# Optimization experiments

Measured on AMD Instinct MI355X. Metric: run time of the kernel, lower is better.

Reference implementation:

```python
import jax, jax.numpy as jnp
import numpy as np

EPS = 1e-5

def setup_inputs() -> dict:
    key = jax.random.key(0)
    k1, k2 = jax.random.split(key)
    N, D, O = 32768, 4096, 256
    x = jax.random.normal(k1, (N, D), dtype=jnp.float32)
    gamma = jnp.ones((D,), dtype=jnp.float32)
    beta = jnp.zeros((D,), dtype=jnp.float32)
    W = jax.random.normal(k2, (O, D), dtype=jnp.float32) * (1.0 / np.sqrt(D))
    b = jnp.zeros((O,), dtype=jnp.float32)
    return {"x": x, "gamma": gamma, "beta": beta, "W": W, "b": b}


def reference(x, gamma, beta, W, b):
    # BatchNorm1d in training mode: per-feature batch mean and biased variance
    mean = jnp.mean(x, axis=0)                      # [D]
    var = jnp.mean(jnp.square(x - mean), axis=0)    # [D], biased (divide by N)
    xhat = (x - mean) * jax.lax.rsqrt(var + EPS)
    h = jax.nn.relu(xhat * gamma + beta)            # [N, D]
    # Linear projection
    return h @ W.T + b                               # [N, O]
```

## Files before the change

kernel.cpp:

```cpp
#include <hip/hip_runtime.h>
#include <hip/hip_bf16.h>

#define NROWS 32768
#define DDIM  4096
#define ODIM  256
#define EPSV  1e-5f

#define CHUNKS 128
#define RPC    256

#define BM 128
#define BK 64
#define NKT (DDIM / BK)

typedef __attribute__((ext_vector_type(4))) float          f32x4;
typedef __attribute__((ext_vector_type(8))) __bf16         bf16x8;
typedef __attribute__((ext_vector_type(8))) unsigned short u16x8;
typedef __attribute__((ext_vector_type(4))) unsigned short u16x4;

static __device__ __forceinline__ unsigned short f2bf(float f) {
  return __builtin_bit_cast(unsigned short, __float2bfloat16(f));
}

__global__ __launch_bounds__(256) void k1_stats(const float* __restrict__ x,
                                                float* __restrict__ psum,
                                                float* __restrict__ psq) {
  const int col = blockIdx.x * 1024 + threadIdx.x * 4;
  const float* p = x + (size_t)blockIdx.y * RPC * DDIM + col;
  f32x4 s = {0.f, 0.f, 0.f, 0.f};
  f32x4 q = {0.f, 0.f, 0.f, 0.f};
#pragma unroll 8
  for (int r = 0; r < RPC; ++r) {
    f32x4 v = *(const f32x4*)p;
    p += DDIM;
    s += v;
    q += v * v;
  }
  *(f32x4*)(psum + (size_t)blockIdx.y * DDIM + col) = s;
  *(f32x4*)(psq  + (size_t)blockIdx.y * DDIM + col) = q;
}

__global__ __launch_bounds__(256) void k2_stats_finalize(
    const float* __restrict__ psum, const float* __restrict__ psq,
    const float* __restrict__ gamma, const float* __restrict__ beta,
    float* __restrict__ scale, float* __restrict__ shift) {
  __shared__ float ss[4][64];
  __shared__ float sq[4][64];
  const int lane = threadIdx.x & 63;
  const int g    = threadIdx.x >> 6;
  const int d    = blockIdx.x * 64 + lane;
  float s = 0.f, qq = 0.f;
  for (int c = g * 32; c < (g + 1) * 32; ++c) {
    s  += psum[(size_t)c * DDIM + d];
    qq += psq [(size_t)c * DDIM + d];
  }
  ss[g][lane] = s;
  sq[g][lane] = qq;
  __syncthreads();
  if (g == 0) {
    s  = ss[0][lane] + ss[1][lane] + ss[2][lane] + ss[3][lane];
    qq = sq[0][lane] + sq[1][lane] + sq[2][lane] + sq[3][lane];
    const float inv = 1.0f / (float)NROWS;
    const float mean = s * inv;
    const float var  = fmaxf(qq * inv - mean * mean, 0.f);
    const float a = gamma[d] * rsqrtf(var + EPSV);
    scale[d] = a;
    shift[d] = beta[d] - mean * a;
  }
}

__global__ __launch_bounds__(256) void k2_wconv(const float* __restrict__ Wf,
                                                unsigned short* __restrict__ Wb) {
  const size_t i = ((size_t)blockIdx.x * 256 + threadIdx.x) * 4;
  f32x4 v = *(const f32x4*)(Wf + i);
  u16x4 o;
  o[0] = f2bf(v[0]); o[1] = f2bf(v[1]); o[2] = f2bf(v[2]); o[3] = f2bf(v[3]);
  *(u16x4*)(Wb + i) = o;
}

__global__ __launch_bounds__(512, 1) void k3_bn_gemm(
    const float* __restrict__ x,
    const unsigned short* __restrict__ Wb,
    const float* __restrict__ scale,
    const float* __restrict__ shift,
    const float* __restrict__ bias,
    float* __restrict__ out) {
  __shared__ unsigned short As[2][BM * BK];
  __shared__ unsigned short Bs[2][ODIM * BK];
  __shared__ float SF[DDIM];
  __shared__ float SH[DDIM];

  const int tid = threadIdx.x;
  const int l   = tid & 63;
  const int w   = tid >> 6;
  const int wr  = w >> 2;
  const int wc  = w & 3;
  const size_t bm0 = (size_t)blockIdx.x * BM;

  ((f32x4*)SF)[tid * 2]     = ((const f32x4*)scale)[tid * 2];
  ((f32x4*)SF)[tid * 2 + 1] = ((const f32x4*)scale)[tid * 2 + 1];
  ((f32x4*)SH)[tid * 2]     = ((const f32x4*)shift)[tid * 2];
  ((f32x4*)SH)[tid * 2 + 1] = ((const f32x4*)shift)[tid * 2 + 1];

  const int rA = tid >> 3;
  const int uA = tid & 7;
  const float* xp0 = x + (bm0 + rA) * (size_t)DDIM + uA * 8;
  const float* xp1 = xp0 + (size_t)64 * DDIM;
  const int awo = rA * 64 + ((uA ^ (rA & 7)) << 3);
  int ktb = uA * 8;

  const unsigned short* bsrc[4];
#pragma unroll
  for (int q = 0; q < 4; ++q) {
    const int p  = w * 256 + q * 64 + l;
    const int o  = p >> 3;
    const int up = p & 7;
    bsrc[q] = Wb + (size_t)o * DDIM + ((up ^ (o & 7)) << 3);
  }

  int offA[4], offB[4];
#pragma unroll
  for (int i = 0; i < 4; ++i) {
    const int row = wr * 64 + i * 16 + (l & 15);
    offA[i] = row * 64 + (((l >> 4) ^ (row & 7)) << 3);
  }
#pragma unroll
  for (int j = 0; j < 4; ++j) {
    const int row = wc * 64 + j * 16 + (l & 15);
    offB[j] = row * 64 + (((l >> 4) ^ (row & 7)) << 3);
  }

  const f32x4 zero = {0.f, 0.f, 0.f, 0.f};
  f32x4 acc[4][4];
#pragma unroll
  for (int i = 0; i < 4; ++i)
#pragma unroll
    for (int j = 0; j < 4; ++j) acc[i][j] = zero;

#define ISSUE_A(V00, V01, V10, V11)                                            \
  asm volatile("global_load_dwordx4 %0, %1, off" : "=v"(V00) : "v"(xp0));      \
  asm volatile("global_load_dwordx4 %0, %1, off" : "=v"(V01) : "v"(xp0 + 4));  \
  asm volatile("global_load_dwordx4 %0, %1, off" : "=v"(V10) : "v"(xp1));      \
  asm volatile("global_load_dwordx4 %0, %1, off" : "=v"(V11) : "v"(xp1 + 4));  \
  asm volatile("" ::: "memory");

#define ISSUE_B(BUFI)                                                          \
  _Pragma("unroll")                                                            \
  for (int q = 0; q < 4; ++q) {                                                \
    __builtin_amdgcn_global_load_lds(                                          \
        (__attribute__((address_space(1))) void*)bsrc[q],                      \
        (__attribute__((address_space(3))) void*)(                             \
            &Bs[BUFI][(w * 256 + q * 64) * 8]),                                \
        16, 0, 0);                                                             \
    bsrc[q] += BK;                                                             \
  }

#define TRANSFORM_WRITE(BUFI, V00, V01, V10, V11)                              \
  {                                                                            \
    f32x4 sa0 = *(const f32x4*)&SF[ktb];                                       \
    f32x4 sa1 = *(const f32x4*)&SF[ktb + 4];                                   \
    f32x4 sc0 = *(const f32x4*)&SH[ktb];                                       \
    f32x4 sc1 = *(const f32x4*)&SH[ktb + 4];                                   \
    ktb += BK;                                                                 \
    u16x8 pk0, pk1;                                                            \
    _Pragma("unroll")                                                          \
    for (int e = 0; e < 4; ++e) {                                              \
      pk0[e]     = f2bf(fmaxf(V00[e] * sa0[e] + sc0[e], 0.f));                 \
      pk0[e + 4] = f2bf(fmaxf(V01[e] * sa1[e] + sc1[e], 0.f));                 \
      pk1[e]     = f2bf(fmaxf(V10[e] * sa0[e] + sc0[e], 0.f));                 \
      pk1[e + 4] = f2bf(fmaxf(V11[e] * sa1[e] + sc1[e], 0.f));                 \
    }                                                                          \
    *(u16x8*)&As[BUFI][awo]        = pk0;                                      \
    *(u16x8*)&As[BUFI][awo + 4096] = pk1;                                      \
  }

#define MFMA_PHASE(BUFI)                                                       \
  _Pragma("unroll")                                                            \
  for (int kk = 0; kk < 2; ++kk) {                                             \
    const int kx = kk << 5;                                                    \
    bf16x8 af[4], bfr[4];                                                      \
    _Pragma("unroll")                                                          \
    for (int i = 0; i < 4; ++i)                                                \
      af[i] = __builtin_bit_cast(bf16x8,                                       \
                                 *(const u16x8*)&As[BUFI][offA[i] ^ kx]);      \
    _Pragma("unroll")                                                          \
    for (int j = 0; j < 4; ++j)                                                \
      bfr[j] = __builtin_bit_cast(bf16x8,                                      \
                                  *(const u16x8*)&Bs[BUFI][offB[j] ^ kx]);     \
    _Pragma("unroll")                                                          \
    for (int i = 0; i < 4; ++i)                                                \
      _Pragma("unroll")                                                        \
      for (int j = 0; j < 4; ++j)                                              \
        acc[i][j] = __builtin_amdgcn_mfma_f32_16x16x32_bf16(                   \
            af[i], bfr[j], acc[i][j], 0, 0, 0);                                \
  }

  {
    f32x4 v00, v01, v10, v11;
    ISSUE_A(v00, v01, v10, v11);
    ISSUE_B(0);
    xp0 += BK; xp1 += BK;
    asm volatile("s_waitcnt lgkmcnt(0)" ::: "memory");
    __builtin_amdgcn_sched_barrier(0);
    __builtin_amdgcn_s_barrier();
    asm volatile("s_waitcnt vmcnt(4)" ::: "memory");
    __builtin_amdgcn_sched_barrier(0);
    TRANSFORM_WRITE(0, v00, v01, v10, v11);
    asm volatile("s_waitcnt vmcnt(0) lgkmcnt(0)" ::: "memory");
    __builtin_amdgcn_sched_barrier(0);
    __builtin_amdgcn_s_barrier();
  }

#define STEP(CUR, PF)                                                          \
  do {                                                                         \
    f32x4 v00, v01, v10, v11;                                                  \
    if (PF) {                                                                  \
      ISSUE_A(v00, v01, v10, v11);                                             \
      ISSUE_B((CUR) ^ 1);                                                      \
      xp0 += BK; xp1 += BK;                                                    \
    }                                                                          \
    MFMA_PHASE(CUR);                                                           \
    if (PF) {                                                                  \
      asm volatile("s_waitcnt vmcnt(4)" ::: "memory");                         \
      __builtin_amdgcn_sched_barrier(0);                                       \
      TRANSFORM_WRITE((CUR) ^ 1, v00, v01, v10, v11);                          \
    }                                                                          \
    asm volatile("s_waitcnt vmcnt(0) lgkmcnt(0)" ::: "memory");                \
    __builtin_amdgcn_sched_barrier(0);                                         \
    __builtin_amdgcn_s_barrier();                                              \
  } while (0)

  for (int kt = 0; kt < NKT - 2; kt += 2) {
    STEP(0, true);
    STEP(1, true);
  }
  STEP(0, true);
  STEP(1, false);
#undef STEP
#undef MFMA_PHASE
#undef TRANSFORM_WRITE
#undef ISSUE_B
#undef ISSUE_A

  const int cl = l & 15;
  const int rg = l >> 4;
#pragma unroll
  for (int j = 0; j < 4; ++j) {
    const int oc = wc * 64 + j * 16 + cl;
    const float bv = bias[oc];
#pragma unroll
    for (int i = 0; i < 4; ++i) {
      const size_t r0 = bm0 + wr * 64 + i * 16 + rg * 4;
#pragma unroll
      for (int rr = 0; rr < 4; ++rr) {
        out[(r0 + rr) * ODIM + oc] = acc[i][j][rr] + bv;
      }
    }
  }
}

extern "C" void kernel_launch(void* const* d_in, const int* in_sizes, int n_in,
                              void* d_out, int out_size, void* d_ws, size_t ws_size,
                              hipStream_t stream) {
  const float* x     = (const float*)d_in[0];
  const float* gamma = (const float*)d_in[1];
  const float* beta  = (const float*)d_in[2];
  const float* W     = (const float*)d_in[3];
  const float* b     = (const float*)d_in[4];
  float* out = (float*)d_out;

  float* psum  = (float*)d_ws;
  float* psq   = psum + (size_t)CHUNKS * DDIM;
  float* scale = psum + 2 * (size_t)CHUNKS * DDIM;
  float* shift = scale + DDIM;
  unsigned short* Wb = (unsigned short*)(shift + DDIM);

  k1_stats<<<dim3(4, CHUNKS), 256, 0, stream>>>(x, psum, psq);
  k2_stats_finalize<<<DDIM / 64, 256, 0, stream>>>(psum, psq, gamma, beta, scale, shift);
  k2_wconv<<<(ODIM * DDIM) / 1024, 256, 0, stream>>>(W, Wb);
  k3_bn_gemm<<<NROWS / BM, 512, 0, stream>>>(x, Wb, scale, shift, b, out);
}
```

Measured before the change: 239.2 us.

## Emit bf16 copy of x during stats pass and feed GEMM from it

```diff
diff --git a/kernel.cpp b/kernel.cpp
--- a/kernel.cpp
+++ b/kernel.cpp
@@ -21,12 +21,18 @@
 static __device__ __forceinline__ unsigned short f2bf(float f) {
   return __builtin_bit_cast(unsigned short, __float2bfloat16(f));
 }
+static __device__ __forceinline__ float bf2f(unsigned short u) {
+  return __builtin_bit_cast(float, ((unsigned)u) << 16);
+}
 
 __global__ __launch_bounds__(256) void k1_stats(const float* __restrict__ x,
                                                 float* __restrict__ psum,
-                                                float* __restrict__ psq) {
+                                                float* __restrict__ psq,
+                                                unsigned short* __restrict__ xb) {
   const int col = blockIdx.x * 1024 + threadIdx.x * 4;
-  const float* p = x + (size_t)blockIdx.y * RPC * DDIM + col;
+  const size_t base = (size_t)blockIdx.y * RPC * DDIM + col;
+  const float* p = x + base;
+  unsigned short* xo = xb + base;
   f32x4 s = {0.f, 0.f, 0.f, 0.f};
   f32x4 q = {0.f, 0.f, 0.f, 0.f};
 #pragma unroll 8
@@ -35,6 +41,10 @@
     p += DDIM;
     s += v;
     q += v * v;
+    u16x4 o;
+    o[0] = f2bf(v[0]); o[1] = f2bf(v[1]); o[2] = f2bf(v[2]); o[3] = f2bf(v[3]);
+    *(u16x4*)xo = o;
+    xo += DDIM;
   }
   *(f32x4*)(psum + (size_t)blockIdx.y * DDIM + col) = s;
   *(f32x4*)(psq  + (size_t)blockIdx.y * DDIM + col) = q;
@@ -79,7 +89,7 @@
 }
 
 __global__ __launch_bounds__(512, 1) void k3_bn_gemm(
-    const float* __restrict__ x,
+    const unsigned short* __restrict__ xb,
     const unsigned short* __restrict__ Wb,
     const float* __restrict__ scale,
     const float* __restrict__ shift,
@@ -87,8 +97,8 @@
     float* __restrict__ out) {
   __shared__ unsigned short As[2][BM * BK];
   __shared__ unsigned short Bs[2][ODIM * BK];
-  __shared__ float SF[DDIM];
-  __shared__ float SH[DDIM];
+  __shared__ unsigned short SFb[DDIM];
+  __shared__ unsigned short SHb[DDIM];
 
   const int tid = threadIdx.x;
   const int l   = tid & 63;
@@ -97,17 +107,29 @@
   const int wc  = w & 3;
   const size_t bm0 = (size_t)blockIdx.x * BM;
 
-  ((f32x4*)SF)[tid * 2]     = ((const f32x4*)scale)[tid * 2];
-  ((f32x4*)SF)[tid * 2 + 1] = ((const f32x4*)scale)[tid * 2 + 1];
-  ((f32x4*)SH)[tid * 2]     = ((const f32x4*)shift)[tid * 2];
-  ((f32x4*)SH)[tid * 2 + 1] = ((const f32x4*)shift)[tid * 2 + 1];
-
-  const int rA = tid >> 3;
-  const int uA = tid & 7;
-  const float* xp0 = x + (bm0 + rA) * (size_t)DDIM + uA * 8;
-  const float* xp1 = xp0 + (size_t)64 * DDIM;
-  const int awo = rA * 64 + ((uA ^ (rA & 7)) << 3);
-  int ktb = uA * 8;
+  {
+    const int c0 = tid * 8;
+    f32x4 s0 = *(const f32x4*)(scale + c0);
+    f32x4 s1 = *(const f32x4*)(scale + c0 + 4);
+    f32x4 h0 = *(const f32x4*)(shift + c0);
+    f32x4 h1 = *(const f32x4*)(shift + c0 + 4);
+    u16x8 os, oh;
+#pragma unroll
+    for (int e = 0; e < 4; ++e) {
+      os[e] = f2bf(s0[e]); os[e + 4] = f2bf(s1[e]);
+      oh[e] = f2bf(h0[e]); oh[e + 4] = f2bf(h1[e]);
+    }
+    *(u16x8*)&SFb[c0] = os;
+    *(u16x8*)&SHb[c0] = oh;
+  }
+
+  const int rA = tid >> 2;
+  const int uA = tid & 3;
+  const unsigned short* xp = xb + (bm0 + rA) * (size_t)DDIM + uA * 16;
+  const int sw = rA & 7;
+  const int aw0 = rA * 64 + (((uA * 2)     ^ sw) << 3);
+  const int aw1 = rA * 64 + (((uA * 2 + 1) ^ sw) << 3);
+  int ktb = uA * 16;
 
   const unsigned short* bsrc[4];
 #pragma unroll
@@ -137,11 +159,10 @@
 #pragma unroll
     for (int j = 0; j < 4; ++j) acc[i][j] = zero;
 
-#define ISSUE_A(V00, V01, V10, V11)                                            \
-  asm volatile("global_load_dwordx4 %0, %1, off" : "=v"(V00) : "v"(xp0));      \
-  asm volatile("global_load_dwordx4 %0, %1, off" : "=v"(V01) : "v"(xp0 + 4));  \
-  asm volatile("global_load_dwordx4 %0, %1, off" : "=v"(V10) : "v"(xp1));      \
-  asm volatile("global_load_dwordx4 %0, %1, off" : "=v"(V11) : "v"(xp1 + 4));  \
+#define ISSUE_A(S0, S1)                                                        \
+  asm volatile("global_load_dwordx4 %0, %1, off" : "=v"(S0) : "v"(xp));        \
+  asm volatile("global_load_dwordx4 %0, %1, off" : "=v"(S1) : "v"(xp + 8));    \
+  xp += BK;                                                                    \
   asm volatile("" ::: "memory");
 
 #define ISSUE_B(BUFI)                                                          \
@@ -153,25 +174,24 @@
             &Bs[BUFI][(w * 256 + q * 64) * 8]),                                \
         16, 0, 0);                                                             \
     bsrc[q] += BK;                                                             \
-  }
-
-#define TRANSFORM_WRITE(BUFI, V00, V01, V10, V11)                              \
+  }                                                                            \
+  asm volatile("" ::: "memory");
+
+#define TRANSFORM_WRITE(BUFI, S0, S1)                                          \
   {                                                                            \
-    f32x4 sa0 = *(const f32x4*)&SF[ktb];                                       \
-    f32x4 sa1 = *(const f32x4*)&SF[ktb + 4];                                   \
-    f32x4 sc0 = *(const f32x4*)&SH[ktb];                                       \
-    f32x4 sc1 = *(const f32x4*)&SH[ktb + 4];                                   \
+    u16x8 a0 = *(const u16x8*)&SFb[ktb];                                       \
+    u16x8 a1 = *(const u16x8*)&SFb[ktb + 8];                                   \
+    u16x8 c0 = *(const u16x8*)&SHb[ktb];                                       \
+    u16x8 c1 = *(const u16x8*)&SHb[ktb + 8];                                   \
     ktb += BK;                                                                 \
     u16x8 pk0, pk1;                                                            \
     _Pragma("unroll")                                                          \
-    for (int e = 0; e < 4; ++e) {                                              \
-      pk0[e]     = f2bf(fmaxf(V00[e] * sa0[e] + sc0[e], 0.f));                 \
-      pk0[e + 4] = f2bf(fmaxf(V01[e] * sa1[e] + sc1[e], 0.f));                 \
-      pk1[e]     = f2bf(fmaxf(V10[e] * sa0[e] + sc0[e], 0.f));                 \
-      pk1[e + 4] = f2bf(fmaxf(V11[e] * sa1[e] + sc1[e], 0.f));                 \
+    for (int e = 0; e < 8; ++e) {                                              \
+      pk0[e] = f2bf(fmaxf(bf2f(S0[e]) * bf2f(a0[e]) + bf2f(c0[e]), 0.f));      \
+      pk1[e] = f2bf(fmaxf(bf2f(S1[e]) * bf2f(a1[e]) + bf2f(c1[e]), 0.f));      \
     }                                                                          \
-    *(u16x8*)&As[BUFI][awo]        = pk0;                                      \
-    *(u16x8*)&As[BUFI][awo + 4096] = pk1;                                      \
+    *(u16x8*)&As[BUFI][aw0] = pk0;                                             \
+    *(u16x8*)&As[BUFI][aw1] = pk1;                                             \
   }
 
 #define MFMA_PHASE(BUFI)                                                       \
@@ -196,16 +216,15 @@
   }
 
   {
-    f32x4 v00, v01, v10, v11;
-    ISSUE_A(v00, v01, v10, v11);
+    u16x8 s0, s1;
+    ISSUE_A(s0, s1);
     ISSUE_B(0);
-    xp0 += BK; xp1 += BK;
     asm volatile("s_waitcnt lgkmcnt(0)" ::: "memory");
     __builtin_amdgcn_sched_barrier(0);
     __builtin_amdgcn_s_barrier();
     asm volatile("s_waitcnt vmcnt(4)" ::: "memory");
     __builtin_amdgcn_sched_barrier(0);
-    TRANSFORM_WRITE(0, v00, v01, v10, v11);
+    TRANSFORM_WRITE(0, s0, s1);
     asm volatile("s_waitcnt vmcnt(0) lgkmcnt(0)" ::: "memory");
     __builtin_amdgcn_sched_barrier(0);
     __builtin_amdgcn_s_barrier();
@@ -213,17 +232,16 @@
 
 #define STEP(CUR, PF)                                                          \
   do {                                                                         \
-    f32x4 v00, v01, v10, v11;                                                  \
+    u16x8 s0, s1;                                                              \
     if (PF) {                                                                  \
-      ISSUE_A(v00, v01, v10, v11);                                             \
+      ISSUE_A(s0, s1);                                                         \
       ISSUE_B((CUR) ^ 1);                                                      \
-      xp0 += BK; xp1 += BK;                                                    \
     }                                                                          \
     MFMA_PHASE(CUR);                                                           \
     if (PF) {                                                                  \
       asm volatile("s_waitcnt vmcnt(4)" ::: "memory");                         \
       __builtin_amdgcn_sched_barrier(0);                                       \
-      TRANSFORM_WRITE((CUR) ^ 1, v00, v01, v10, v11);                          \
+      TRANSFORM_WRITE((CUR) ^ 1, s0, s1);                                      \
     }                                                                          \
     asm volatile("s_waitcnt vmcnt(0) lgkmcnt(0)" ::: "memory");                \
     __builtin_amdgcn_sched_barrier(0);                                         \
@@ -269,14 +287,15 @@
   const float* b     = (const float*)d_in[4];
   float* out = (float*)d_out;
 
-  float* psum  = (float*)d_ws;
+  unsigned short* xbw = (unsigned short*)d_ws;
+  float* psum  = (float*)(xbw + (size_t)NROWS * DDIM);
   float* psq   = psum + (size_t)CHUNKS * DDIM;
-  float* scale = psum + 2 * (size_t)CHUNKS * DDIM;
+  float* scale = psq  + (size_t)CHUNKS * DDIM;
   float* shift = scale + DDIM;
   unsigned short* Wb = (unsigned short*)(shift + DDIM);
 
-  k1_stats<<<dim3(4, CHUNKS), 256, 0, stream>>>(x, psum, psq);
+  k1_stats<<<dim3(4, CHUNKS), 256, 0, stream>>>(x, psum, psq, xbw);
   k2_stats_finalize<<<DDIM / 64, 256, 0, stream>>>(psum, psq, gamma, beta, scale, shift);
   k2_wconv<<<(ODIM * DDIM) / 1024, 256, 0, stream>>>(W, Wb);
-  k3_bn_gemm<<<NROWS / BM, 512, 0, stream>>>(x, Wb, scale, shift, b, out);
-}
+  k3_bn_gemm<<<NROWS / BM, 512, 0, stream>>>(xbw, Wb, scale, shift, b, out);
+}
```

Measured after the change: 281.1 us. 17.5% more time.

## Split GEMM output columns across two blocks with XCD-aware mapping and bf16 BN params

Applied to the files above, without the earlier changes.

```diff
diff --git a/kernel.cpp b/kernel.cpp
--- a/kernel.cpp
+++ b/kernel.cpp
@@ -10,6 +10,7 @@
 #define RPC    256
 
 #define BM 128
+#define BN 128
 #define BK 64
 #define NKT (DDIM / BK)
 
@@ -20,6 +21,9 @@
 
 static __device__ __forceinline__ unsigned short f2bf(float f) {
   return __builtin_bit_cast(unsigned short, __float2bfloat16(f));
+}
+static __device__ __forceinline__ float bf2f(unsigned short u) {
+  return __builtin_bit_cast(float, ((unsigned)u) << 16);
 }
 
 __global__ __launch_bounds__(256) void k1_stats(const float* __restrict__ x,
@@ -40,82 +44,91 @@
   *(f32x4*)(psq  + (size_t)blockIdx.y * DDIM + col) = q;
 }
 
-__global__ __launch_bounds__(256) void k2_stats_finalize(
+__global__ __launch_bounds__(256) void k2_finalize_wconv(
     const float* __restrict__ psum, const float* __restrict__ psq,
     const float* __restrict__ gamma, const float* __restrict__ beta,
-    float* __restrict__ scale, float* __restrict__ shift) {
-  __shared__ float ss[4][64];
-  __shared__ float sq[4][64];
-  const int lane = threadIdx.x & 63;
-  const int g    = threadIdx.x >> 6;
-  const int d    = blockIdx.x * 64 + lane;
-  float s = 0.f, qq = 0.f;
-  for (int c = g * 32; c < (g + 1) * 32; ++c) {
-    s  += psum[(size_t)c * DDIM + d];
-    qq += psq [(size_t)c * DDIM + d];
-  }
-  ss[g][lane] = s;
-  sq[g][lane] = qq;
-  __syncthreads();
-  if (g == 0) {
-    s  = ss[0][lane] + ss[1][lane] + ss[2][lane] + ss[3][lane];
-    qq = sq[0][lane] + sq[1][lane] + sq[2][lane] + sq[3][lane];
-    const float inv = 1.0f / (float)NROWS;
-    const float mean = s * inv;
-    const float var  = fmaxf(qq * inv - mean * mean, 0.f);
-    const float a = gamma[d] * rsqrtf(var + EPSV);
-    scale[d] = a;
-    shift[d] = beta[d] - mean * a;
-  }
-}
-
-__global__ __launch_bounds__(256) void k2_wconv(const float* __restrict__ Wf,
-                                                unsigned short* __restrict__ Wb) {
-  const size_t i = ((size_t)blockIdx.x * 256 + threadIdx.x) * 4;
-  f32x4 v = *(const f32x4*)(Wf + i);
-  u16x4 o;
-  o[0] = f2bf(v[0]); o[1] = f2bf(v[1]); o[2] = f2bf(v[2]); o[3] = f2bf(v[3]);
-  *(u16x4*)(Wb + i) = o;
-}
-
-__global__ __launch_bounds__(512, 1) void k3_bn_gemm(
+    const float* __restrict__ Wf,
+    unsigned short* __restrict__ ssb, unsigned short* __restrict__ shb,
+    unsigned short* __restrict__ Wb) {
+  if (blockIdx.x < 64) {
+    __shared__ float ss[4][64];
+    __shared__ float sq[4][64];
+    const int lane = threadIdx.x & 63;
+    const int g    = threadIdx.x >> 6;
+    const int d    = blockIdx.x * 64 + lane;
+    float s = 0.f, qq = 0.f;
+    for (int c = g * 32; c < (g + 1) * 32; ++c) {
+      s  += psum[(size_t)c * DDIM + d];
+      qq += psq [(size_t)c * DDIM + d];
+    }
+    ss[g][lane] = s;
+    sq[g][lane] = qq;
+    __syncthreads();
+    if (g == 0) {
+      s  = ss[0][lane] + ss[1][lane] + ss[2][lane] + ss[3][lane];
+      qq = sq[0][lane] + sq[1][lane] + sq[2][lane] + sq[3][lane];
+      const float inv = 1.0f / (float)NROWS;
+      const float mean = s * inv;
+      const float var  = fmaxf(qq * inv - mean * mean, 0.f);
+      const float a = gamma[d] * rsqrtf(var + EPSV);
+      ssb[d] = f2bf(a);
+      shb[d] = f2bf(beta[d] - mean * a);
+    }
+  } else {
+    const size_t i = ((size_t)(blockIdx.x - 64) * 256 + threadIdx.x) * 4;
+    f32x4 v = *(const f32x4*)(Wf + i);
+    u16x4 o;
+    o[0] = f2bf(v[0]); o[1] = f2bf(v[1]); o[2] = f2bf(v[2]); o[3] = f2bf(v[3]);
+    *(u16x4*)(Wb + i) = o;
+  }
+}
+
+__global__ __launch_bounds__(256, 2) void k3_bn_gemm(
     const float* __restrict__ x,
     const unsigned short* __restrict__ Wb,
-    const float* __restrict__ scale,
-    const float* __restrict__ shift,
+    const unsigned short* __restrict__ ssg,
+    const unsigned short* __restrict__ shg,
     const float* __restrict__ bias,
     float* __restrict__ out) {
   __shared__ unsigned short As[2][BM * BK];
-  __shared__ unsigned short Bs[2][ODIM * BK];
-  __shared__ float SF[DDIM];
-  __shared__ float SH[DDIM];
+  __shared__ unsigned short Bs[2][BN * BK];
+  __shared__ unsigned short SFb[DDIM];
+  __shared__ unsigned short SHb[DDIM];
 
   const int tid = threadIdx.x;
   const int l   = tid & 63;
   const int w   = tid >> 6;
-  const int wr  = w >> 2;
-  const int wc  = w & 3;
-  const size_t bm0 = (size_t)blockIdx.x * BM;
-
-  ((f32x4*)SF)[tid * 2]     = ((const f32x4*)scale)[tid * 2];
-  ((f32x4*)SF)[tid * 2 + 1] = ((const f32x4*)scale)[tid * 2 + 1];
-  ((f32x4*)SH)[tid * 2]     = ((const f32x4*)shift)[tid * 2];
-  ((f32x4*)SH)[tid * 2 + 1] = ((const f32x4*)shift)[tid * 2 + 1];
-
-  const int rA = tid >> 3;
-  const int uA = tid & 7;
-  const float* xp0 = x + (bm0 + rA) * (size_t)DDIM + uA * 8;
-  const float* xp1 = xp0 + (size_t)64 * DDIM;
-  const int awo = rA * 64 + ((uA ^ (rA & 7)) << 3);
-  int ktb = uA * 8;
+  const int wr  = w >> 1;
+  const int wc  = w & 1;
+  const int b   = blockIdx.x;
+  const int xcd = b & 7;
+  const int j8  = b >> 3;
+  const int m   = xcd * 32 + (j8 >> 1);
+  const int nh  = j8 & 1;
+  const size_t bm0 = (size_t)m * BM;
+  const int ncol0  = nh * BN;
+
+  {
+    const int c0 = tid * 16;
+    *(u16x8*)&SFb[c0]     = *(const u16x8*)(ssg + c0);
+    *(u16x8*)&SFb[c0 + 8] = *(const u16x8*)(ssg + c0 + 8);
+    *(u16x8*)&SHb[c0]     = *(const u16x8*)(shg + c0);
+    *(u16x8*)&SHb[c0 + 8] = *(const u16x8*)(shg + c0 + 8);
+  }
+
+  const int rA = tid >> 1;
+  const int h  = tid & 1;
+  const float* xq = x + (bm0 + rA) * (size_t)DDIM + h * 32;
+  const int sw = rA & 7;
+  int ktb = h * 32;
 
   const unsigned short* bsrc[4];
 #pragma unroll
   for (int q = 0; q < 4; ++q) {
-    const int p  = w * 256 + q * 64 + l;
+    const int p  = q * 256 + tid;
     const int o  = p >> 3;
     const int up = p & 7;
-    bsrc[q] = Wb + (size_t)o * DDIM + ((up ^ (o & 7)) << 3);
+    bsrc[q] = Wb + (size_t)(ncol0 + o) * DDIM + ((up ^ (o & 7)) << 3);
   }
 
   int offA[4], offB[4];
@@ -125,9 +138,9 @@
     offA[i] = row * 64 + (((l >> 4) ^ (row & 7)) << 3);
   }
 #pragma unroll
-  for (int j = 0; j < 4; ++j) {
-    const int row = wc * 64 + j * 16 + (l & 15);
-    offB[j] = row * 64 + (((l >> 4) ^ (row & 7)) << 3);
+  for (int jj = 0; jj < 4; ++jj) {
+    const int row = wc * 64 + jj * 16 + (l & 15);
+    offB[jj] = row * 64 + (((l >> 4) ^ (row & 7)) << 3);
   }
 
   const f32x4 zero = {0.f, 0.f, 0.f, 0.f};
@@ -135,13 +148,18 @@
 #pragma unroll
   for (int i = 0; i < 4; ++i)
 #pragma unroll
-    for (int j = 0; j < 4; ++j) acc[i][j] = zero;
-
-#define ISSUE_A(V00, V01, V10, V11)                                            \
-  asm volatile("global_load_dwordx4 %0, %1, off" : "=v"(V00) : "v"(xp0));      \
-  asm volatile("global_load_dwordx4 %0, %1, off" : "=v"(V01) : "v"(xp0 + 4));  \
-  asm volatile("global_load_dwordx4 %0, %1, off" : "=v"(V10) : "v"(xp1));      \
-  asm volatile("global_load_dwordx4 %0, %1, off" : "=v"(V11) : "v"(xp1 + 4));  \
+    for (int jj = 0; jj < 4; ++jj) acc[i][jj] = zero;
+
+#define ISSUE_A(S)                                                             \
+  asm volatile("global_load_dwordx4 %0, %1, off"            : "=v"(S[0]) : "v"(xq)); \
+  asm volatile("global_load_dwordx4 %0, %1, off offset:16"  : "=v"(S[1]) : "v"(xq)); \
+  asm volatile("global_load_dwordx4 %0, %1, off offset:32"  : "=v"(S[2]) : "v"(xq)); \
+  asm volatile("global_load_dwordx4 %0, %1, off offset:48"  : "=v"(S[3]) : "v"(xq)); \
+  asm volatile("global_load_dwordx4 %0, %1, off offset:64"  : "=v"(S[4]) : "v"(xq)); \
+  asm volatile("global_load_dwordx4 %0, %1, off offset:80"  : "=v"(S[5]) : "v"(xq)); \
+  asm volatile("global_load_dwordx4 %0, %1, off offset:96"  : "=v"(S[6]) : "v"(xq)); \
+  asm volatile("global_load_dwordx4 %0, %1, off offset:112" : "=v"(S[7]) : "v"(xq)); \
+  xq += BK;                                                                    \
   asm volatile("" ::: "memory");
 
 #define ISSUE_B(BUFI)                                                          \
@@ -150,31 +168,31 @@
     __builtin_amdgcn_global_load_lds(                                          \
         (__attribute__((address_space(1))) void*)bsrc[q],                      \
         (__attribute__((address_space(3))) void*)(                             \
-            &Bs[BUFI][(w * 256 + q * 64) * 8]),                                \
+            &Bs[BUFI][(q * 256 + (tid & ~63)) * 8]),                           \
         16, 0, 0);                                                             \
     bsrc[q] += BK;                                                             \
-  }
-
-#define TRANSFORM_WRITE(BUFI, V00, V01, V10, V11)                              \
+  }                                                                            \
+  asm volatile("" ::: "memory");
+
+#define TRANSFORM_WRITE(BUFI, S)                                               \
   {                                                                            \
-    f32x4 sa0 = *(const f32x4*)&SF[ktb];                                       \
-    f32x4 sa1 = *(const f32x4*)&SF[ktb + 4];                                   \
-    f32x4 sc0 = *(const f32x4*)&SH[ktb];                                       \
-    f32x4 sc1 = *(const f32x4*)&SH[ktb + 4];                                   \
+    _Pragma("unroll")                                                          \
+    for (int u = 0; u < 4; ++u) {                                              \
+      u16x8 av = *(const u16x8*)&SFb[ktb + u * 8];                             \
+      u16x8 cv = *(const u16x8*)&SHb[ktb + u * 8];                             \
+      u16x8 pk;                                                                \
+      _Pragma("unroll")                                                        \
+      for (int e = 0; e < 4; ++e) {                                            \
+        pk[e]     = f2bf(fmaxf(S[2 * u][e]     * bf2f(av[e])     + bf2f(cv[e]),     0.f)); \
+        pk[e + 4] = f2bf(fmaxf(S[2 * u + 1][e] * bf2f(av[e + 4]) + bf2f(cv[e + 4]), 0.f)); \
+      }                                                                        \
+      *(u16x8*)&As[BUFI][rA * 64 + (((h * 4 + u) ^ sw) << 3)] = pk;            \
+    }                                                                          \
     ktb += BK;                                                                 \
-    u16x8 pk0, pk1;                                                            \
-    _Pragma("unroll")                                                          \
-    for (int e = 0; e < 4; ++e) {                                              \
-      pk0[e]     = f2bf(fmaxf(V00[e] * sa0[e] + sc0[e], 0.f));                 \
-      pk0[e + 4] = f2bf(fmaxf(V01[e] * sa1[e] + sc1[e], 0.f));                 \
-      pk1[e]     = f2bf(fmaxf(V10[e] * sa0[e] + sc0[e], 0.f));                 \
-      pk1[e + 4] = f2bf(fmaxf(V11[e] * sa1[e] + sc1[e], 0.f));                 \
-    }                                                                          \
-    *(u16x8*)&As[BUFI][awo]        = pk0;                                      \
-    *(u16x8*)&As[BUFI][awo + 4096] = pk1;                                      \
   }
 
 #define MFMA_PHASE(BUFI)                                                       \
+  __builtin_amdgcn_s_setprio(1);                                              \
   _Pragma("unroll")                                                            \
   for (int kk = 0; kk < 2; ++kk) {                                             \
     const int kx = kk << 5;                                                    \
@@ -184,28 +202,28 @@
       af[i] = __builtin_bit_cast(bf16x8,                                       \
                                  *(const u16x8*)&As[BUFI][offA[i] ^ kx]);      \
     _Pragma("unroll")                                                          \
-    for (int j = 0; j < 4; ++j)                                                \
-      bfr[j] = __builtin_bit_cast(bf16x8,                                      \
-                                  *(const u16x8*)&Bs[BUFI][offB[j] ^ kx]);     \
+    for (int jj = 0; jj < 4; ++jj)                                             \
+      bfr[jj] = __builtin_bit_cast(bf16x8,                                     \
+                                   *(const u16x8*)&Bs[BUFI][offB[jj] ^ kx]);   \
     _Pragma("unroll")                                                          \
     for (int i = 0; i < 4; ++i)                                                \
       _Pragma("unroll")                                                        \
-      for (int j = 0; j < 4; ++j)                                              \
-        acc[i][j] = __builtin_amdgcn_mfma_f32_16x16x32_bf16(                   \
-            af[i], bfr[j], acc[i][j], 0, 0, 0);                                \
-  }
+      for (int jj = 0; jj < 4; ++jj)                                           \
+        acc[i][jj] = __builtin_amdgcn_mfma_f32_16x16x32_bf16(                  \
+            af[i], bfr[jj], acc[i][jj], 0, 0, 0);                              \
+  }                                                                            \
+  __builtin_amdgcn_s_setprio(0);
 
   {
-    f32x4 v00, v01, v10, v11;
-    ISSUE_A(v00, v01, v10, v11);
+    f32x4 S[8];
+    ISSUE_A(S);
     ISSUE_B(0);
-    xp0 += BK; xp1 += BK;
     asm volatile("s_waitcnt lgkmcnt(0)" ::: "memory");
     __builtin_amdgcn_sched_barrier(0);
     __builtin_amdgcn_s_barrier();
     asm volatile("s_waitcnt vmcnt(4)" ::: "memory");
     __builtin_amdgcn_sched_barrier(0);
-    TRANSFORM_WRITE(0, v00, v01, v10, v11);
+    TRANSFORM_WRITE(0, S);
     asm volatile("s_waitcnt vmcnt(0) lgkmcnt(0)" ::: "memory");
     __builtin_amdgcn_sched_barrier(0);
     __builtin_amdgcn_s_barrier();
@@ -213,17 +231,16 @@
 
 #define STEP(CUR, PF)                                                          \
   do {                                                                         \
-    f32x4 v00, v01, v10, v11;                                                  \
+    f32x4 S[8];                                                                \
     if (PF) {                                                                  \
-      ISSUE_A(v00, v01, v10, v11);                                             \
+      ISSUE_A(S);                                                              \
       ISSUE_B((CUR) ^ 1);                                                      \
-      xp0 += BK; xp1 += BK;                                                    \
     }                                                                          \
     MFMA_PHASE(CUR);                                                           \
     if (PF) {                                                                  \
       asm volatile("s_waitcnt vmcnt(4)" ::: "memory");                         \
       __builtin_amdgcn_sched_barrier(0);                                       \
-      TRANSFORM_WRITE((CUR) ^ 1, v00, v01, v10, v11);                          \
+      TRANSFORM_WRITE((CUR) ^ 1, S);                                           \
     }                                                                          \
     asm volatile("s_waitcnt vmcnt(0) lgkmcnt(0)" ::: "memory");                \
     __builtin_amdgcn_sched_barrier(0);                                         \
@@ -245,15 +262,15 @@
   const int cl = l & 15;
   const int rg = l >> 4;
 #pragma unroll
-  for (int j = 0; j < 4; ++j) {
-    const int oc = wc * 64 + j * 16 + cl;
+  for (int jj = 0; jj < 4; ++jj) {
+    const int oc = ncol0 + wc * 64 + jj * 16 + cl;
     const float bv = bias[oc];
 #pragma unroll
     for (int i = 0; i < 4; ++i) {
       const size_t r0 = bm0 + wr * 64 + i * 16 + rg * 4;
 #pragma unroll
       for (int rr = 0; rr < 4; ++rr) {
-        out[(r0 + rr) * ODIM + oc] = acc[i][j][rr] + bv;
+        out[(r0 + rr) * ODIM + oc] = acc[i][jj][rr] + bv;
       }
     }
   }
@@ -271,12 +288,12 @@
 
   float* psum  = (float*)d_ws;
   float* psq   = psum + (size_t)CHUNKS * DDIM;
-  float* scale = psum + 2 * (size_t)CHUNKS * DDIM;
-  float* shift = scale + DDIM;
-  unsigned short* Wb = (unsigned short*)(shift + DDIM);
+  unsigned short* Wb  = (unsigned short*)(psq + (size_t)CHUNKS * DDIM);
+  unsigned short* ssb = Wb + (size_t)ODIM * DDIM;
+  unsigned short* shb = ssb + DDIM;
 
   k1_stats<<<dim3(4, CHUNKS), 256, 0, stream>>>(x, psum, psq);
-  k2_stats_finalize<<<DDIM / 64, 256, 0, stream>>>(psum, psq, gamma, beta, scale, shift);
-  k2_wconv<<<(ODIM * DDIM) / 1024, 256, 0, stream>>>(W, Wb);
-  k3_bn_gemm<<<NROWS / BM, 512, 0, stream>>>(x, Wb, scale, shift, b, out);
-}
+  k2_finalize_wconv<<<64 + (ODIM * DDIM) / 1024, 256, 0, stream>>>(
+      psum, psq, gamma, beta, W, ssb, shb, Wb);
+  k3_bn_gemm<<<(NROWS / BM) * 2, 256, 0, stream>>>(x, Wb, ssb, shb, b, out);
+}
```

After: 301.3 us. 26.0% more time.
